# Optimization experiments

Hardware: AMD Instinct MI355X
Metric: run time of the kernel (lower is better)

The kernel has to match this reference:

```python
import jax, jax.numpy as jnp
import numpy as np
from jax import lax

T, B, D = 2048, 64, 512

def setup_inputs() -> dict:
    key = jax.random.key(0)
    k1, k2 = jax.random.split(key)
    input_x = jax.random.normal(k1, (T, B, D), dtype=jnp.float32)
    # Linear(D+1 -> 1): columns [:D] act on x_t, column [D] acts on z_{t-1}
    W = jax.random.normal(k2, (D + 1,), dtype=jnp.float32) * (1.0 / np.sqrt(D + 1))
    b = jnp.zeros((), dtype=jnp.float32)
    return {"input_x": input_x, "W": W, "b": b}

def reference(input_x, W, b):
    Wx = W[:-1]          # [D] weights for x_t
    wz = W[-1]           # scalar weight for recurrent z
    # Batch the expensive projection outside the recurrence: [T, B]
    xproj = jnp.einsum('tbd,d->tb', input_x, Wx) + b

    def step(z, xp):
        # z: [B], xp: [B]
        z_new = jax.nn.sigmoid(xp + wz * z)
        return z_new, z_new

    z0 = jnp.zeros((input_x.shape[1],), dtype=input_x.dtype)
    _, outs = lax.scan(step, z0, xproj)
    return outs  # [T, B] (matches torch output after squeeze_)
```

## Files before the change

### kernel.cpp

```cpp
#include <hip/hip_runtime.h>
#include <hip/hip_bf16.h>

#define TT 2048
#define BB 64
#define DD 512

__global__ __launch_bounds__(256) void proj_kernel(
    const float* __restrict__ x,
    const float* __restrict__ W,
    const float* __restrict__ bptr,
    float* __restrict__ s_out)
{
    const int lane = threadIdx.x & 63;
    const int wave_id = (blockIdx.x * blockDim.x + threadIdx.x) >> 6;

    const float4 w0 = ((const float4*)W)[lane];
    const float4 w1 = ((const float4*)W)[64 + lane];
    const float bias = *bptr;
    const float NEG_LOG2E = -1.4426950408889634f;

    const int row0 = wave_id * 16;
    const float4* xr = (const float4*)(x + (size_t)row0 * DD);

    float4 ca0 = xr[lane],        ca1 = xr[64 + lane];
    float4 cb0 = xr[128 + lane],  cb1 = xr[192 + lane];

    #pragma unroll
    for (int r = 0; r < 16; r += 2) {
        float4 na0 = ca0, na1 = ca1, nb0 = cb0, nb1 = cb1;
        if (r + 2 < 16) {
            na0 = xr[(r + 2) * 128 + lane];
            na1 = xr[(r + 2) * 128 + 64 + lane];
            nb0 = xr[(r + 3) * 128 + lane];
            nb1 = xr[(r + 3) * 128 + 64 + lane];
        }
        float d0 = ca0.x * w0.x + ca0.y * w0.y + ca0.z * w0.z + ca0.w * w0.w
                 + ca1.x * w1.x + ca1.y * w1.y + ca1.z * w1.z + ca1.w * w1.w;
        float d1 = cb0.x * w0.x + cb0.y * w0.y + cb0.z * w0.z + cb0.w * w0.w
                 + cb1.x * w1.x + cb1.y * w1.y + cb1.z * w1.z + cb1.w * w1.w;
        #pragma unroll
        for (int off = 32; off >= 1; off >>= 1) {
            d0 += __shfl_xor(d0, off, 64);
            d1 += __shfl_xor(d1, off, 64);
        }
        if (lane < 2)
            s_out[row0 + r + lane] = NEG_LOG2E * ((lane ? d1 : d0) + bias);
        ca0 = na0; ca1 = na1; cb0 = nb0; cb1 = nb1;
    }
}

__global__ __launch_bounds__(64, 1) void scan_kernel(
    const float* __restrict__ s,
    const float* __restrict__ W,
    float* __restrict__ out)
{
    const int lane = threadIdx.x;
    const int ch = blockIdx.x;
    const int t0 = ch * 64;
    const float c = -1.4426950408889634f * W[DD];
    const float* sl = s + lane;
    float* ol = out + lane;

    float warm[16];
    float buf[64];
    if (ch > 0) {
        #pragma unroll
        for (int i = 0; i < 16; ++i) warm[i] = sl[(t0 - 16 + i) * BB];
    }
    #pragma unroll
    for (int i = 0; i < 64; ++i) buf[i] = sl[(t0 + i) * BB];

    float z = 0.f;
    if (ch > 0) {
        z = 0.5f;
        #pragma unroll
        for (int i = 0; i < 16; ++i)
            z = __builtin_amdgcn_rcpf(1.f + __builtin_amdgcn_exp2f(fmaf(c, z, warm[i])));
    }

    float zb[64];
    #pragma unroll
    for (int i = 0; i < 64; ++i) {
        z = __builtin_amdgcn_rcpf(1.f + __builtin_amdgcn_exp2f(fmaf(c, z, buf[i])));
        zb[i] = z;
    }
    #pragma unroll
    for (int i = 0; i < 64; ++i) ol[(t0 + i) * BB] = zb[i];
}

extern "C" void kernel_launch(void* const* d_in, const int* in_sizes, int n_in,
                              void* d_out, int out_size, void* d_ws, size_t ws_size,
                              hipStream_t stream) {
    const float* x = (const float*)d_in[0];
    const float* W = (const float*)d_in[1];
    const float* b = (const float*)d_in[2];
    float* out = (float*)d_out;
    float* s = (float*)d_ws;

    proj_kernel<<<2048, 256, 0, stream>>>(x, W, b, s);
    scan_kernel<<<32, 64, 0, stream>>>(s, W, out);
}
```

Before: 357.6 us.

## Fuse projection and scan into one kernel with per-chunk atomic readiness counters

Merges the projection and scan kernels into one launch. Projection blocks bump per-chunk counters with release atomics once their rows are written, and 32 extra scan blocks spin-wait on their chunk's counter, so each scan chunk can start before the whole projection finishes. The scan loop also streams its inputs in groups of eight and writes each output as it is computed, instead of buffering all 64. The design adds a memset launch and relies on scan blocks (highest block indices) being scheduled only after the producer blocks, otherwise spinning blocks could hold resources; the scan tail still runs after most projection work.

```diff
diff --git a/kernel.cpp b/kernel.cpp
--- a/kernel.cpp
+++ b/kernel.cpp
@@ -1,91 +1,114 @@
 #include <hip/hip_runtime.h>
-#include <hip/hip_bf16.h>
 
 #define TT 2048
 #define BB 64
 #define DD 512
+#define NCHUNK (TT / 64)
 
-__global__ __launch_bounds__(256) void proj_kernel(
+__global__ __launch_bounds__(256) void fused_kernel(
     const float* __restrict__ x,
     const float* __restrict__ W,
     const float* __restrict__ bptr,
-    float* __restrict__ s_out)
+    float* __restrict__ s_out,
+    unsigned int* __restrict__ ctr,
+    float* __restrict__ out)
 {
-    const int lane = threadIdx.x & 63;
-    const int wave_id = (blockIdx.x * blockDim.x + threadIdx.x) >> 6;
-
-    const float4 w0 = ((const float4*)W)[lane];
-    const float4 w1 = ((const float4*)W)[64 + lane];
-    const float bias = *bptr;
+    const int blk = blockIdx.x;
     const float NEG_LOG2E = -1.4426950408889634f;
 
-    const int row0 = wave_id * 16;
-    const float4* xr = (const float4*)(x + (size_t)row0 * DD);
+    if (blk < TT) {
+        const int lane = threadIdx.x & 63;
+        const int wave = threadIdx.x >> 6;
 
-    float4 ca0 = xr[lane],        ca1 = xr[64 + lane];
-    float4 cb0 = xr[128 + lane],  cb1 = xr[192 + lane];
+        const float4 w0 = ((const float4*)W)[lane];
+        const float4 w1 = ((const float4*)W)[64 + lane];
+        const float bias = *bptr;
 
-    #pragma unroll
-    for (int r = 0; r < 16; r += 2) {
-        float4 na0 = ca0, na1 = ca1, nb0 = cb0, nb1 = cb1;
-        if (r + 2 < 16) {
-            na0 = xr[(r + 2) * 128 + lane];
-            na1 = xr[(r + 2) * 128 + 64 + lane];
-            nb0 = xr[(r + 3) * 128 + lane];
-            nb1 = xr[(r + 3) * 128 + 64 + lane];
+        const int row0 = blk * BB + wave * 16;
+        const float4* xr = (const float4*)(x + (size_t)row0 * DD);
+
+        float4 ca0 = xr[lane],        ca1 = xr[64 + lane];
+        float4 cb0 = xr[128 + lane],  cb1 = xr[192 + lane];
+
+        #pragma unroll
+        for (int r = 0; r < 16; r += 2) {
+            float4 na0 = ca0, na1 = ca1, nb0 = cb0, nb1 = cb1;
+            if (r + 2 < 16) {
+                na0 = xr[(r + 2) * 128 + lane];
+                na1 = xr[(r + 2) * 128 + 64 + lane];
+                nb0 = xr[(r + 3) * 128 + lane];
+                nb1 = xr[(r + 3) * 128 + 64 + lane];
+            }
+            float d0 = ca0.x * w0.x + ca0.y * w0.y + ca0.z * w0.z + ca0.w * w0.w
+                     + ca1.x * w1.x + ca1.y * w1.y + ca1.z * w1.z + ca1.w * w1.w;
+            float d1 = cb0.x * w0.x + cb0.y * w0.y + cb0.z * w0.z + cb0.w * w0.w
+                     + cb1.x * w1.x + cb1.y * w1.y + cb1.z * w1.z + cb1.w * w1.w;
+            #pragma unroll
+            for (int off = 32; off >= 1; off >>= 1) {
+                d0 += __shfl_xor(d0, off, 64);
+                d1 += __shfl_xor(d1, off, 64);
+            }
+            if (lane < 2)
+                s_out[row0 + r + lane] = NEG_LOG2E * ((lane ? d1 : d0) + bias);
+            ca0 = na0; ca1 = na1; cb0 = nb0; cb1 = nb1;
         }
-        float d0 = ca0.x * w0.x + ca0.y * w0.y + ca0.z * w0.z + ca0.w * w0.w
-                 + ca1.x * w1.x + ca1.y * w1.y + ca1.z * w1.z + ca1.w * w1.w;
-        float d1 = cb0.x * w0.x + cb0.y * w0.y + cb0.z * w0.z + cb0.w * w0.w
-                 + cb1.x * w1.x + cb1.y * w1.y + cb1.z * w1.z + cb1.w * w1.w;
+
+        __threadfence();
+        __syncthreads();
+        if (threadIdx.x == 0) {
+            __hip_atomic_fetch_add(&ctr[blk >> 6], 1u,
+                                   __ATOMIC_RELEASE, __HIP_MEMORY_SCOPE_AGENT);
+            if ((blk & 63) >= 48)
+                __hip_atomic_fetch_add(&ctr[(blk >> 6) + 1], 1u,
+                                       __ATOMIC_RELEASE, __HIP_MEMORY_SCOPE_AGENT);
+        }
+    } else {
+        if (threadIdx.x >= 64) return;
+        const int ch = blk - TT;
+        const int lane = threadIdx.x;
+        const int t0 = ch * 64;
+        const unsigned int need = ch ? 80u : 64u;
+
+        unsigned int v;
+        do {
+            v = __hip_atomic_load(&ctr[ch], __ATOMIC_RELAXED, __HIP_MEMORY_SCOPE_AGENT);
+            if (v < need) __builtin_amdgcn_s_sleep(2);
+        } while (v < need);
+        (void)__hip_atomic_load(&ctr[ch], __ATOMIC_ACQUIRE, __HIP_MEMORY_SCOPE_AGENT);
+
+        const float c = NEG_LOG2E * W[DD];
+        const float* sl = s_out + lane;
+        float* ol = out + lane;
+
+        float z = 0.f;
+        if (ch > 0) {
+            float warm[16];
+            #pragma unroll
+            for (int i = 0; i < 16; ++i) warm[i] = sl[(t0 - 16 + i) * BB];
+            z = 0.5f;
+            #pragma unroll
+            for (int i = 0; i < 16; ++i)
+                z = __builtin_amdgcn_rcpf(1.f + __builtin_amdgcn_exp2f(fmaf(c, z, warm[i])));
+        }
+
+        float cur[8], nxt[8];
         #pragma unroll
-        for (int off = 32; off >= 1; off >>= 1) {
-            d0 += __shfl_xor(d0, off, 64);
-            d1 += __shfl_xor(d1, off, 64);
+        for (int i = 0; i < 8; ++i) cur[i] = sl[(t0 + i) * BB];
+        #pragma unroll
+        for (int g = 0; g < 8; ++g) {
+            if (g < 7) {
+                #pragma unroll
+                for (int i = 0; i < 8; ++i) nxt[i] = sl[(t0 + (g + 1) * 8 + i) * BB];
+            }
+            #pragma unroll
+            for (int i = 0; i < 8; ++i) {
+                z = __builtin_amdgcn_rcpf(1.f + __builtin_amdgcn_exp2f(fmaf(c, z, cur[i])));
+                ol[(t0 + g * 8 + i) * BB] = z;
+            }
+            #pragma unroll
+            for (int i = 0; i < 8; ++i) cur[i] = nxt[i];
         }
-        if (lane < 2)
-            s_out[row0 + r + lane] = NEG_LOG2E * ((lane ? d1 : d0) + bias);
-        ca0 = na0; ca1 = na1; cb0 = nb0; cb1 = nb1;
     }
-}
-
-__global__ __launch_bounds__(64, 1) void scan_kernel(
-    const float* __restrict__ s,
-    const float* __restrict__ W,
-    float* __restrict__ out)
-{
-    const int lane = threadIdx.x;
-    const int ch = blockIdx.x;
-    const int t0 = ch * 64;
-    const float c = -1.4426950408889634f * W[DD];
-    const float* sl = s + lane;
-    float* ol = out + lane;
-
-    float warm[16];
-    float buf[64];
-    if (ch > 0) {
-        #pragma unroll
-        for (int i = 0; i < 16; ++i) warm[i] = sl[(t0 - 16 + i) * BB];
-    }
-    #pragma unroll
-    for (int i = 0; i < 64; ++i) buf[i] = sl[(t0 + i) * BB];
-
-    float z = 0.f;
-    if (ch > 0) {
-        z = 0.5f;
-        #pragma unroll
-        for (int i = 0; i < 16; ++i)
-            z = __builtin_amdgcn_rcpf(1.f + __builtin_amdgcn_exp2f(fmaf(c, z, warm[i])));
-    }
-
-    float zb[64];
-    #pragma unroll
-    for (int i = 0; i < 64; ++i) {
-        z = __builtin_amdgcn_rcpf(1.f + __builtin_amdgcn_exp2f(fmaf(c, z, buf[i])));
-        zb[i] = z;
-    }
-    #pragma unroll
-    for (int i = 0; i < 64; ++i) ol[(t0 + i) * BB] = zb[i];
 }
 
 extern "C" void kernel_launch(void* const* d_in, const int* in_sizes, int n_in,
@@ -96,7 +119,8 @@
     const float* b = (const float*)d_in[2];
     float* out = (float*)d_out;
     float* s = (float*)d_ws;
+    unsigned int* ctr = (unsigned int*)((char*)d_ws + (size_t)TT * BB * sizeof(float));
 
-    proj_kernel<<<2048, 256, 0, stream>>>(x, W, b, s);
-    scan_kernel<<<32, 64, 0, stream>>>(s, W, out);
+    hipMemsetAsync(ctr, 0, (NCHUNK + 1) * sizeof(unsigned int), stream);
+    fused_kernel<<<TT + NCHUNK, 256, 0, stream>>>(x, W, b, s, ctr, out);
 }
```

Measured after the change: 809.8 us. 126% more time.
